# Kernel tuning notes

Measured on AMD Instinct MI355X. Metric: run time of the kernel, lower is better.

The kernel has to match this reference:

```python
import jax, jax.numpy as jnp
import numpy as np

V = 32            # number_variables
K = 16            # degree + 1 spline coefficients per pair
DEG = 3           # cubic B-spline order for basis evaluation
LO, HI = -5.0, 5.0
SPAN_FACTOR = 0.1
N_SAMPLES = 131072
P_PAIRS = V * (V - 1) // 2  # 496


def bspline_basis(x):
    """Cubic B-spline basis with K clamped-uniform basis functions on the
    span_factor-expanded range [LO - s, HI + s].  x: [N] -> [N, K]."""
    s = SPAN_FACTOR * (HI - LO)
    lo, hi = LO - s, HI + s
    n_break = K - DEG + 1
    inner = jnp.linspace(lo, hi, n_break)
    t = jnp.concatenate([jnp.full((DEG,), lo), inner, jnp.full((DEG,), hi)])  # [K+DEG+1]
    x = jnp.clip(x, lo, hi - 1e-6 * (hi - lo))
    xb = x[:, None]
    # order-0 indicator functions: [N, K+DEG]
    B = ((xb >= t[None, :-1]) & (xb < t[None, 1:])).astype(x.dtype)
    for r in range(1, DEG + 1):
        tl, tr = t[:-(r + 1)], t[r:-1]
        den1 = tr - tl
        left = jnp.where(den1 > 0, (xb - tl) / jnp.where(den1 > 0, den1, 1.0), 0.0)
        tl2, tr2 = t[1:-r], t[r + 1:]
        den2 = tr2 - tl2
        right = jnp.where(den2 > 0, (tr2 - xb) / jnp.where(den2 > 0, den2, 1.0), 0.0)
        B = left * B[:, :-1] + right * B[:, 1:]
    return B  # [N, K]


def setup_inputs() -> dict:
    key = jax.random.key(0)
    k1, k2 = jax.random.split(key)
    inp = jax.random.normal(k1, (N_SAMPLES, V), dtype=jnp.float32)
    # learned spline coefficients, one column per (var, covar) pair,
    # initialized near the module's 0.1 constant init
    params = 0.1 + 0.05 * jax.random.normal(k2, (K, P_PAIRS), dtype=jnp.float32)
    return {"input": inp, "params": params}


def reference(input, params):
    # output[:, v] = input[:, v] + sum_{c < v} lambda_{v,c}(input[:, c]) * input[:, c]
    # In forward (non-inverse) mode every lambda depends only on `input`, so all
    # V*(V-1)/2 pairs are computed in one batched contraction instead of a loop.
    Basis = jax.vmap(bspline_basis)(input.T)  # [V, N, K], basis per covariate column
    idx_v, idx_c = np.tril_indices(V, -1)      # pair order matches params_index = v*(v-1)/2 + c
    P_mat = jnp.zeros((V, K, V), dtype=input.dtype).at[idx_c, :, idx_v].set(params.T)
    contrib = jnp.einsum('cnk,ckv->cnv', Basis, P_mat)   # lambda_{v,c}(x_{n,c})
    out = input + jnp.einsum('cnv,nc->nv', contrib, input)
    return out
```

## Files before the change

kernel.cpp:

```cpp
#include <hip/hip_runtime.h>
#include <hip/hip_bf16.h>


#define PPAIR 496

typedef _Float16 f16x8 __attribute__((ext_vector_type(8)));
typedef float f32x4 __attribute__((ext_vector_type(4)));
typedef unsigned int u32;
typedef unsigned int u32x4 __attribute__((ext_vector_type(4)));

__global__ __launch_bounds__(256) void prep_w2t(const float* __restrict__ params,
                                                unsigned short* __restrict__ w2t) {
    int idx = blockIdx.x * 256 + threadIdx.x;
    int v = idx >> 9;
    int c = (idx >> 4) & 31, k = idx & 15;
    float w = 0.0f;
    if (c < v) w = params[k * PPAIR + (v * (v - 1)) / 2 + c];
    _Float16 h = (_Float16)w;
    w2t[idx] = __builtin_bit_cast(unsigned short, h);
}

__global__ __launch_bounds__(256, 4) void decor_main(const float* __restrict__ xin,
                                                     const unsigned short* __restrict__ w2t,
                                                     float* __restrict__ out) {
    const int tid = threadIdx.x;
    const int wv = tid >> 6;
    const int l = tid & 63;
    const int s = l & 15;
    const int q = l >> 4;
    const int qp = q & 1;
    const int sigma = ((q & 1) << 1) | (q >> 1);

    f16x8 b1[8][2];
    f16x8 b0[4][2];
#pragma unroll
    for (int u = 0; u < 8; ++u) {
#pragma unroll
        for (int e = 0; e < 2; ++e) {
            int t = 2 * u + (qp ? (1 - e) : e);
            b1[u][e] = *(const f16x8*)(w2t + (16 + s) * 512 + t * 32 + q * 8);
            if (u < 4) b0[u][e] = *(const f16x8*)(w2t + s * 512 + t * 32 + q * 8);
        }
    }

    const float sc = 13.0f / 12.0f;
    const int S0w = blockIdx.x * 128 + wv * 32;

    float xv[8];
    {
        const float* xr = xin + (S0w + s) * 32 + sigma;
#pragma unroll
        for (int u = 0; u < 8; ++u) xv[u] = xr[4 * u];
    }

#pragma unroll
    for (int tile = 0; tile < 2; ++tile) {
        const int T0 = S0w + tile * 16;

        float xe0[4], xe1[4];
#pragma unroll
        for (int rI = 0; rI < 4; ++rI) {
            int base = (T0 + q * 4 + rI) * 32;
            xe0[rI] = xin[base + s];
            xe1[rI] = xin[base + 16 + s];
        }
        float xvn[8];
        if (tile < 1) {
            const float* xr = xin + (T0 + 16 + s) * 32 + sigma;
#pragma unroll
            for (int u = 0; u < 8; ++u) xvn[u] = xr[4 * u];
        }

        f32x4 acc0 = {0.f, 0.f, 0.f, 0.f};
        f32x4 acc1 = {0.f, 0.f, 0.f, 0.f};

#pragma unroll
        for (int u = 0; u < 8; ++u) {
            float x = xv[u];
            float uu = fmaf(x, sc, 6.5f);
            uu = fminf(fmaxf(uu, 0.0f), 12.999987f);
            int mi = (int)uu;
            float mf = (float)mi;
            float r = uu - mf;
            float N0, N1, N2, N3;
            if (__all(mi >= 3 && mi <= 9)) {
                float omr = 1.0f - r;
                float r2 = r * r, r3 = r2 * r;
                float o2 = omr * omr;
                N0 = o2 * omr * (1.0f / 6.0f);
                N3 = r3 * (1.0f / 6.0f);
                N1 = fmaf(0.5f, r3, (2.0f / 3.0f) - r2);
                N2 = 1.0f - N0 - N1 - N3;
            } else {
                float t13 = 13.0f - mf;
                float af = fminf(mf, 1.0f);
                float bf = fminf(mf, 2.0f);
                float cf = fminf(t13, 2.0f);
                float df = fminf(t13, 3.0f);
                float r1 = 1.0f - r;
                float l2 = r + af, rr2 = cf - r;
                float l3 = r + bf, rr3 = df - r;
                float iv = (af == 0.0f) ? 1.0f : 0.5f;
                float T = r1 * iv;
                float M0 = r1 * T;
                float sv = l2 * T;
                float iv2 = (cf == 1.0f) ? 1.0f : 0.5f;
                float T2 = r * iv2;
                float M1 = fmaf(rr2, T2, sv);
                float M2 = r * T2;
                float iv3 = 0.5f;
                iv3 = (bf == 0.0f) ? 1.0f : iv3;
                iv3 = (bf == 2.0f) ? (1.0f / 3.0f) : iv3;
                T = M0 * iv3;
                N0 = r1 * T;
                sv = l3 * T;
                float g14 = af + cf;
                float iv4 = (g14 == 2.0f) ? 0.5f : (1.0f / 3.0f);
                T = M1 * iv4;
                N1 = fmaf(rr2, T, sv);
                sv = l2 * T;
                float iv5 = 0.5f;
                iv5 = (df == 1.0f) ? 1.0f : iv5;
                iv5 = (df == 3.0f) ? (1.0f / 3.0f) : iv5;
                T = M2 * iv5;
                N2 = fmaf(rr3, T, sv);
                N3 = r * T;
            }
            float g0 = x * N0, g1 = x * N1, g2 = x * N2, g3 = x * N3;
            int e = mi & 1;
            float aa = e ? 0.0f : g0, bb = e ? g0 : g1;
            float cc = e ? g1 : g2, dd = e ? g2 : g3;
            float ee = e ? g3 : 0.0f;
            u32 p0 = __builtin_bit_cast(u32, __builtin_amdgcn_cvt_pkrtz(aa, bb));
            u32 p1 = __builtin_bit_cast(u32, __builtin_amdgcn_cvt_pkrtz(cc, dd));
            u32 p2 = __builtin_bit_cast(u32, __builtin_amdgcn_cvt_pkrtz(ee, 0.0f));
            int w0 = mi >> 1;
            int dlt = w0 & 1;
            u32 C0 = dlt ? 0u : p0;
            u32 C1 = dlt ? p0 : p1;
            u32 C2 = dlt ? p1 : p2;
            u32 C3 = dlt ? p2 : 0u;
            int j0 = (w0 & 6) ^ (qp << 2);
            bool b2 = (j0 & 2) != 0;
            u32 t0 = b2 ? 0u : C0;
            u32 t1 = b2 ? 0u : C1;
            u32 t2 = b2 ? C0 : C2;
            u32 t3 = b2 ? C1 : C3;
            u32 t4 = b2 ? C2 : 0u;
            u32 t5 = b2 ? C3 : 0u;
            bool b4 = (j0 & 4) != 0;
            u32 B0 = b4 ? t4 : t0;
            u32 B1 = b4 ? t5 : t1;
            u32 B2 = b4 ? 0u : t2;
            u32 B3 = b4 ? 0u : t3;
            u32 B4 = b4 ? t0 : t4;
            u32 B5 = b4 ? t1 : t5;
            u32 B6 = b4 ? t2 : 0u;
            u32 B7 = b4 ? t3 : 0u;
            u32 R0 = (u32)__shfl_xor((int)B4, 16);
            u32 R1 = (u32)__shfl_xor((int)B5, 16);
            u32 R2 = (u32)__shfl_xor((int)B6, 16);
            u32 R3 = (u32)__shfl_xor((int)B7, 16);
            u32x4 kp = {B0, B1, B2, B3};
            u32x4 rc = {R0, R1, R2, R3};
            f16x8 ka = __builtin_bit_cast(f16x8, kp);
            f16x8 ra = __builtin_bit_cast(f16x8, rc);
            acc1 = __builtin_amdgcn_mfma_f32_16x16x32_f16(ka, b1[u][0], acc1, 0, 0, 0);
            acc1 = __builtin_amdgcn_mfma_f32_16x16x32_f16(ra, b1[u][1], acc1, 0, 0, 0);
            if (u < 4) {
                acc0 = __builtin_amdgcn_mfma_f32_16x16x32_f16(ka, b0[u][0], acc0, 0, 0, 0);
                acc0 = __builtin_amdgcn_mfma_f32_16x16x32_f16(ra, b0[u][1], acc0, 0, 0, 0);
            }
        }

#pragma unroll
        for (int rI = 0; rI < 4; ++rI) {
            int sample = T0 + q * 4 + rI;
            int base = sample * 32;
            out[base + s]      = xe0[rI] + acc0[rI];
            out[base + 16 + s] = xe1[rI] + acc1[rI];
        }

        if (tile < 1) {
#pragma unroll
            for (int u = 0; u < 8; ++u) xv[u] = xvn[u];
        }
    }
}

extern "C" void kernel_launch(void* const* d_in, const int* in_sizes, int n_in,
                              void* d_out, int out_size, void* d_ws, size_t ws_size,
                              hipStream_t stream) {
    const float* xin = (const float*)d_in[0];
    const float* params = (const float*)d_in[1];
    float* out = (float*)d_out;
    unsigned short* w2t = (unsigned short*)d_ws;

    prep_w2t<<<64, 256, 0, stream>>>(params, w2t);
    decor_main<<<1024, 256, 0, stream>>>(xin, w2t, out);
}
```

Measured before the change: 90.64 us.

## Split covariate range across wave pairs and reduce partial sums via LDS

Each pair of waves now shares a 16-sample tile, with each wave handling half of the covariate columns (u range). The second-half wave's partial accumulator is combined through shared memory, so per-wave register pressure and serial MFMA chains shrink. The grid doubles to 2048 blocks. The cost is a __syncthreads per tile, LDS traffic, and load imbalance, since h==1 waves skip the acc0 MFMAs. The prep kernel's write indexing was also rewritten.

```diff
diff --git a/kernel.cpp b/kernel.cpp
--- a/kernel.cpp
+++ b/kernel.cpp
@@ -11,71 +11,76 @@
 
 __global__ __launch_bounds__(256) void prep_w2t(const float* __restrict__ params,
                                                 unsigned short* __restrict__ w2t) {
-    int idx = blockIdx.x * 256 + threadIdx.x;
-    int v = idx >> 9;
-    int c = (idx >> 4) & 31, k = idx & 15;
+    int i = blockIdx.x * 256 + threadIdx.x;
+    int c = i & 31;
+    int k = (i >> 5) & 15;
+    int v = i >> 9;
     float w = 0.0f;
     if (c < v) w = params[k * PPAIR + (v * (v - 1)) / 2 + c];
     _Float16 h = (_Float16)w;
-    w2t[idx] = __builtin_bit_cast(unsigned short, h);
+    w2t[v * 512 + c * 16 + k] = __builtin_bit_cast(unsigned short, h);
 }
 
 __global__ __launch_bounds__(256, 4) void decor_main(const float* __restrict__ xin,
                                                      const unsigned short* __restrict__ w2t,
                                                      float* __restrict__ out) {
+    __shared__ float P[2][2][16 * 17];
+
     const int tid = threadIdx.x;
     const int wv = tid >> 6;
+    const int h = wv & 1;
+    const int pair = wv >> 1;
     const int l = tid & 63;
     const int s = l & 15;
     const int q = l >> 4;
     const int qp = q & 1;
-    const int sigma = ((q & 1) << 1) | (q >> 1);
-
-    f16x8 b1[8][2];
-    f16x8 b0[4][2];
-#pragma unroll
-    for (int u = 0; u < 8; ++u) {
+    const int qh = q >> 1;
+    const int sigma = 2 * qp + qh;
+
+    f16x8 bA[4][2];
+    f16x8 bB[4][2];
+    const int tb = 8 * h;
+#pragma unroll
+    for (int u = 0; u < 4; ++u) {
 #pragma unroll
         for (int e = 0; e < 2; ++e) {
-            int t = 2 * u + (qp ? (1 - e) : e);
-            b1[u][e] = *(const f16x8*)(w2t + (16 + s) * 512 + t * 32 + q * 8);
-            if (u < 4) b0[u][e] = *(const f16x8*)(w2t + s * 512 + t * 32 + q * 8);
+            int t = tb + 2 * u + (qp ? (1 - e) : e);
+            bA[u][e] = *(const f16x8*)(w2t + (16 + s) * 512 + t * 32 + q * 8);
+            if (h == 0) bB[u][e] = *(const f16x8*)(w2t + s * 512 + t * 32 + q * 8);
         }
     }
 
     const float sc = 13.0f / 12.0f;
-    const int S0w = blockIdx.x * 128 + wv * 32;
-
-    float xv[8];
+    const int Tbase = blockIdx.x * 64 + pair * 16;
+
+    float xv[4];
     {
-        const float* xr = xin + (S0w + s) * 32 + sigma;
-#pragma unroll
-        for (int u = 0; u < 8; ++u) xv[u] = xr[4 * u];
+        const float* xr = xin + (Tbase + s) * 32 + 16 * h + sigma;
+#pragma unroll
+        for (int u = 0; u < 4; ++u) xv[u] = xr[4 * u];
     }
 
 #pragma unroll
-    for (int tile = 0; tile < 2; ++tile) {
-        const int T0 = S0w + tile * 16;
-
-        float xe0[4], xe1[4];
-#pragma unroll
-        for (int rI = 0; rI < 4; ++rI) {
-            int base = (T0 + q * 4 + rI) * 32;
-            xe0[rI] = xin[base + s];
-            xe1[rI] = xin[base + 16 + s];
-        }
-        float xvn[8];
-        if (tile < 1) {
-            const float* xr = xin + (T0 + 16 + s) * 32 + sigma;
-#pragma unroll
-            for (int u = 0; u < 8; ++u) xvn[u] = xr[4 * u];
+    for (int i = 0; i < 2; ++i) {
+        const int T0 = Tbase + i * 32;
+
+        float xe[4];
+#pragma unroll
+        for (int rI = 0; rI < 4; ++rI)
+            xe[rI] = xin[(T0 + q * 4 + rI) * 32 + 16 * h + s];
+
+        float xvn[4];
+        if (i == 0) {
+            const float* xr = xin + (Tbase + 32 + s) * 32 + 16 * h + sigma;
+#pragma unroll
+            for (int u = 0; u < 4; ++u) xvn[u] = xr[4 * u];
         }
 
         f32x4 acc0 = {0.f, 0.f, 0.f, 0.f};
         f32x4 acc1 = {0.f, 0.f, 0.f, 0.f};
 
 #pragma unroll
-        for (int u = 0; u < 8; ++u) {
+        for (int u = 0; u < 4; ++u) {
             float x = xv[u];
             float uu = fmaf(x, sc, 6.5f);
             uu = fminf(fmaxf(uu, 0.0f), 12.999987f);
@@ -165,25 +170,34 @@
             u32x4 rc = {R0, R1, R2, R3};
             f16x8 ka = __builtin_bit_cast(f16x8, kp);
             f16x8 ra = __builtin_bit_cast(f16x8, rc);
-            acc1 = __builtin_amdgcn_mfma_f32_16x16x32_f16(ka, b1[u][0], acc1, 0, 0, 0);
-            acc1 = __builtin_amdgcn_mfma_f32_16x16x32_f16(ra, b1[u][1], acc1, 0, 0, 0);
-            if (u < 4) {
-                acc0 = __builtin_amdgcn_mfma_f32_16x16x32_f16(ka, b0[u][0], acc0, 0, 0, 0);
-                acc0 = __builtin_amdgcn_mfma_f32_16x16x32_f16(ra, b0[u][1], acc0, 0, 0, 0);
+            acc1 = __builtin_amdgcn_mfma_f32_16x16x32_f16(ka, bA[u][0], acc1, 0, 0, 0);
+            acc1 = __builtin_amdgcn_mfma_f32_16x16x32_f16(ra, bA[u][1], acc1, 0, 0, 0);
+            if (h == 0) {
+                acc0 = __builtin_amdgcn_mfma_f32_16x16x32_f16(ka, bB[u][0], acc0, 0, 0, 0);
+                acc0 = __builtin_amdgcn_mfma_f32_16x16x32_f16(ra, bB[u][1], acc0, 0, 0, 0);
             }
         }
 
+        if (h == 0) {
+#pragma unroll
+            for (int rI = 0; rI < 4; ++rI)
+                P[i][pair][(q * 4 + rI) * 17 + s] = acc1[rI];
+        }
+        __syncthreads();
+
 #pragma unroll
         for (int rI = 0; rI < 4; ++rI) {
-            int sample = T0 + q * 4 + rI;
-            int base = sample * 32;
-            out[base + s]      = xe0[rI] + acc0[rI];
-            out[base + 16 + s] = xe1[rI] + acc1[rI];
-        }
-
-        if (tile < 1) {
-#pragma unroll
-            for (int u = 0; u < 8; ++u) xv[u] = xvn[u];
+            int bo = (T0 + q * 4 + rI) * 32;
+            if (h == 0) {
+                out[bo + s] = xe[rI] + acc0[rI];
+            } else {
+                out[bo + 16 + s] = xe[rI] + acc1[rI] + P[i][pair][(q * 4 + rI) * 17 + s];
+            }
+        }
+
+        if (i == 0) {
+#pragma unroll
+            for (int u = 0; u < 4; ++u) xv[u] = xvn[u];
         }
     }
 }
@@ -197,5 +211,5 @@
     unsigned short* w2t = (unsigned short*)d_ws;
 
     prep_w2t<<<64, 256, 0, stream>>>(params, w2t);
-    decor_main<<<1024, 256, 0, stream>>>(xin, w2t, out);
+    decor_main<<<2048, 256, 0, stream>>>(xin, w2t, out);
 }
```

New measurement: 90.14 us. About the same (-0.5%).
